# Kernel tuning notes

Hardware: AMD Instinct MI355X
Metric: run time of the kernel (lower is better)

The kernel has to match this reference:

```python
import jax, jax.numpy as jnp
import numpy as np

BIN_NUM = 20
BIN_WIDTH = 0.1
FEAT_MAP_NUM = 64


def setup_inputs() -> dict:
    key = jax.random.key(0)
    kx, kw, kb = jax.random.split(key, 3)
    B, C, H, W = 16, FEAT_MAP_NUM, 256, 256
    x = jax.random.normal(kx, (B, C, H, W), dtype=jnp.float32)
    # Faithful MTLU init: weight zeros for negative half-bins, ones for positive;
    # small noise added so the baseline exercises non-trivial per-bin values.
    half = BIN_NUM // 2
    w0 = jnp.concatenate(
        [jnp.zeros((C, half), jnp.float32), jnp.ones((C, BIN_NUM - half), jnp.float32)],
        axis=1,
    )
    mtluweight = w0 + 0.05 * jax.random.normal(kw, (C, BIN_NUM), dtype=jnp.float32)
    mtlubias = 0.05 * jax.random.normal(kb, (C, BIN_NUM), dtype=jnp.float32)
    return {"x": x, "mtluweight": mtluweight, "mtlubias": mtlubias}


def _mtlu(x, weight, bias):
    # per-element bin index: floor(x / BinWidth) + BinNum/2, clamped to [0, BinNum-1]
    idx = jnp.clip(
        jnp.floor(x * (1.0 / BIN_WIDTH)).astype(jnp.int32) + BIN_NUM // 2,
        0,
        BIN_NUM - 1,
    )  # [B,C,H,W] int32
    C = weight.shape[0]
    ch = jnp.arange(C, dtype=jnp.int32)[None, :, None, None]  # broadcast channel index
    w = weight[ch, idx]  # [B,C,H,W] gather per (channel, bin)
    b = bias[ch, idx]
    return w * x + b


def reference(x, mtluweight, mtlubias):
    tmp = _mtlu(x, mtluweight, mtlubias)
    return tmp * jax.nn.sigmoid(x)
```

## Files before the change

### kernel.cpp

```cpp
#include <hip/hip_runtime.h>
#include <hip/hip_bf16.h>


#define MT_C 64
#define MT_BINS 20
#define MT_TABLE (MT_C * MT_BINS)


__global__ __launch_bounds__(256) void mtsilu_kernel(
    const float4* __restrict__ x,
    const float* __restrict__ weight,
    const float* __restrict__ bias,
    float4* __restrict__ out,
    int nvec)
{
    __shared__ float sw[MT_TABLE];
    __shared__ float sb[MT_TABLE];
    for (int i = threadIdx.x; i < MT_TABLE; i += 256) {
        sw[i] = weight[i];
        sb[i] = bias[i];
    }
    __syncthreads();

    const int stride = gridDim.x * 256;
    for (int i = blockIdx.x * 256 + threadIdx.x; i < nvec; i += stride) {
        float4 v = x[i];
        const int cbase = ((i >> 14) & (MT_C - 1)) * MT_BINS;

        float r[4];
        float xv[4] = {v.x, v.y, v.z, v.w};
        #pragma unroll
        for (int k = 0; k < 4; ++k) {
            float xk = xv[k];
            int idx = (int)floorf(xk * 10.0f) + (MT_BINS / 2);
            idx = idx < 0 ? 0 : (idx > MT_BINS - 1 ? MT_BINS - 1 : idx);
            float wv = sw[cbase + idx];
            float bv = sb[cbase + idx];
            float s = 1.0f / (1.0f + __expf(-xk));
            r[k] = (wv * xk + bv) * s;
        }
        float4 o;
        o.x = r[0]; o.y = r[1]; o.z = r[2]; o.w = r[3];
        out[i] = o;
    }
}

extern "C" void kernel_launch(void* const* d_in, const int* in_sizes, int n_in,
                              void* d_out, int out_size, void* d_ws, size_t ws_size,
                              hipStream_t stream) {
    const float4* x      = (const float4*)d_in[0];
    const float*  weight = (const float*)d_in[1];
    const float*  bias   = (const float*)d_in[2];
    float4*       out    = (float4*)d_out;

    const int n    = in_sizes[0];
    const int nvec = n / 4;

    const int block = 256;
    const int grid  = 16384;
    mtsilu_kernel<<<grid, block, 0, stream>>>(x, weight, bias, out, nvec);
}
```

Before: 434.6 us.

## Assign fixed per-channel chunks to blocks with per-channel LUT and unrolled loads

Each block now handles one quarter of a single channel plane, so it loads only that channel's 20 weight/bias pairs into shared memory as float2, replacing the full 64-channel table. Each thread processes 16 float4s with four loads issued before any compute, which adds memory-level parallelism. The sigmoid reciprocal uses the hardware rcp intrinsic and the bin index uses a round-down conversion. The grid-stride loop is gone, so the grid now has one block per chunk, and a guarded tail path covers partial final chunks.

```diff
diff --git a/kernel.cpp b/kernel.cpp
--- a/kernel.cpp
+++ b/kernel.cpp
@@ -1,47 +1,70 @@
 #include <hip/hip_runtime.h>
-#include <hip/hip_bf16.h>
 
 
-#define MT_C 64
 #define MT_BINS 20
-#define MT_TABLE (MT_C * MT_BINS)
+#define NTHREADS 256
+#define PLANE_VEC 16384
+#define BPP 4
+#define CHUNK (PLANE_VEC / BPP)
+#define ITERS (CHUNK / NTHREADS)
+#define UNROLL 4
 
+__device__ __forceinline__ float mtsilu_elem(float xk,
+                                             const float2* __restrict__ swb) {
+    int idx = __float2int_rd(xk * 10.0f) + (MT_BINS / 2);
+    idx = idx < 0 ? 0 : (idx > MT_BINS - 1 ? MT_BINS - 1 : idx);
+    float2 t = swb[idx];
+    float s = __builtin_amdgcn_rcpf(1.0f + __expf(-xk));
+    return fmaf(t.x, xk, t.y) * s;
+}
 
-__global__ __launch_bounds__(256) void mtsilu_kernel(
+__global__ __launch_bounds__(NTHREADS) void mtsilu_kernel(
     const float4* __restrict__ x,
     const float* __restrict__ weight,
     const float* __restrict__ bias,
     float4* __restrict__ out,
     int nvec)
 {
-    __shared__ float sw[MT_TABLE];
-    __shared__ float sb[MT_TABLE];
-    for (int i = threadIdx.x; i < MT_TABLE; i += 256) {
-        sw[i] = weight[i];
-        sb[i] = bias[i];
+    __shared__ float2 swb[MT_BINS];
+    const int c = ((int)blockIdx.x / BPP) & 63;
+    if (threadIdx.x < MT_BINS) {
+        swb[threadIdx.x] = make_float2(weight[c * MT_BINS + threadIdx.x],
+                                       bias[c * MT_BINS + threadIdx.x]);
     }
     __syncthreads();
 
-    const int stride = gridDim.x * 256;
-    for (int i = blockIdx.x * 256 + threadIdx.x; i < nvec; i += stride) {
-        float4 v = x[i];
-        const int cbase = ((i >> 14) & (MT_C - 1)) * MT_BINS;
+    const int base = (int)blockIdx.x * CHUNK + (int)threadIdx.x;
 
-        float r[4];
-        float xv[4] = {v.x, v.y, v.z, v.w};
+    if ((int)blockIdx.x != (int)gridDim.x - 1 || base + (ITERS - 1) * NTHREADS < nvec) {
         #pragma unroll
-        for (int k = 0; k < 4; ++k) {
-            float xk = xv[k];
-            int idx = (int)floorf(xk * 10.0f) + (MT_BINS / 2);
-            idx = idx < 0 ? 0 : (idx > MT_BINS - 1 ? MT_BINS - 1 : idx);
-            float wv = sw[cbase + idx];
-            float bv = sb[cbase + idx];
-            float s = 1.0f / (1.0f + __expf(-xk));
-            r[k] = (wv * xk + bv) * s;
+        for (int it = 0; it < ITERS; it += UNROLL) {
+            float4 v[UNROLL];
+            #pragma unroll
+            for (int u = 0; u < UNROLL; ++u)
+                v[u] = x[base + (it + u) * NTHREADS];
+            #pragma unroll
+            for (int u = 0; u < UNROLL; ++u) {
+                float4 o;
+                o.x = mtsilu_elem(v[u].x, swb);
+                o.y = mtsilu_elem(v[u].y, swb);
+                o.z = mtsilu_elem(v[u].z, swb);
+                o.w = mtsilu_elem(v[u].w, swb);
+                out[base + (it + u) * NTHREADS] = o;
+            }
         }
-        float4 o;
-        o.x = r[0]; o.y = r[1]; o.z = r[2]; o.w = r[3];
-        out[i] = o;
+    } else {
+        for (int it = 0; it < ITERS; ++it) {
+            int j = base + it * NTHREADS;
+            if (j < nvec) {
+                float4 v = x[j];
+                float4 o;
+                o.x = mtsilu_elem(v.x, swb);
+                o.y = mtsilu_elem(v.y, swb);
+                o.z = mtsilu_elem(v.z, swb);
+                o.w = mtsilu_elem(v.w, swb);
+                out[j] = o;
+            }
+        }
     }
 }
 
@@ -56,7 +79,6 @@
     const int n    = in_sizes[0];
     const int nvec = n / 4;
 
-    const int block = 256;
-    const int grid  = 16384;
-    mtsilu_kernel<<<grid, block, 0, stream>>>(x, weight, bias, out, nvec);
+    const int grid = (nvec + CHUNK - 1) / CHUNK;
+    mtsilu_kernel<<<grid, NTHREADS, 0, stream>>>(x, weight, bias, out, nvec);
 }
```

Result: no change. 429.7 us (-1.1%).
